# Kernel optimization log

Hardware: AMD Instinct MI355X
Metric: run time of the kernel (lower is better)

## Reference

```python
import jax, jax.numpy as jnp
import numpy as np

N = 100000      # nodes
MUL_IN = 256    # multiplicity of 0e and 1o in irreps_in ('256x0e + 256x1o')
MUL_H = 64      # multiplicity in MLP_irreps ('64x0e + 64x1o')
# irreps_nonlin = (64+64)x0e (scalars + gates) + 64x1o (gated)


def setup_inputs() -> dict:
    key = jax.random.key(0)
    k0, k1, k2, k3, k4 = jax.random.split(key, 5)
    # e3nn flat layout: [scalars (256), vectors (256*3, as (mul,3) flattened)]
    x = jax.random.normal(k0, (N, MUL_IN * 4), dtype=jnp.float32)
    # linear_1 block weights (e3nn Linear: randn init, output scaled by 1/sqrt(fan_in))
    w1_s = jax.random.normal(k1, (MUL_IN, 2 * MUL_H), dtype=jnp.float32)  # 0e->0e (scalars+gates)
    w1_v = jax.random.normal(k2, (MUL_IN, MUL_H), dtype=jnp.float32)      # 1o->1o
    # linear_2 block weights: 64x0e->1x0e, 64x1o->1x1o
    w2_s = jax.random.normal(k3, (MUL_H, 1), dtype=jnp.float32)
    w2_v = jax.random.normal(k4, (MUL_H, 1), dtype=jnp.float32)
    return {"x": x, "w1_s": w1_s, "w1_v": w1_v, "w2_s": w2_s, "w2_v": w2_v}


def reference(x, w1_s, w1_v, w2_s, w2_v):
    # ---- split input into irrep blocks ----
    xs = x[:, :MUL_IN]                          # [N, 256] 0e scalars
    xv = x[:, MUL_IN:].reshape(-1, MUL_IN, 3)   # [N, 256, 3] 1o vectors

    inv_in = np.float32(1.0 / np.sqrt(MUL_IN))
    # ---- linear_1: per-irrep block-diagonal matmuls (weight shared over m) ----
    h_s = (xs @ w1_s) * inv_in                              # [N, 128] scalars+gates
    h_v = jnp.einsum('nmi,mk->nki', xv, w1_v) * inv_in       # [N, 64, 3]

    # ---- Gate: act(scalars), act(gates) * gated_vectors ----
    scalars = h_s[:, :MUL_H]
    gates = h_s[:, MUL_H:]
    g_s = jax.nn.silu(scalars)                               # [N, 64]
    g_v = jax.nn.silu(gates)[:, :, None] * h_v               # [N, 64, 3]

    inv_h = np.float32(1.0 / np.sqrt(MUL_H))
    # ---- linear_2: 64x0e -> 1x0e, 64x1o -> 1x1o ----
    out_s = (g_s @ w2_s) * inv_h                             # [N, 1]
    out_v = jnp.einsum('nmi,mk->nki', g_v, w2_v).reshape(-1, 3) * inv_h  # [N, 3]
    return jnp.concatenate([out_s, out_v], axis=1)           # [N, 4] = 1x0e + 1x1o
```

## Files before the change

### kernel.cpp

```cpp
#include <hip/hip_runtime.h>
#include <hip/hip_bf16.h>
#include <math.h>

#define N_ROWS  100000
#define NT_ROW  6250

typedef __attribute__((ext_vector_type(8))) short bf16x8;
typedef __attribute__((ext_vector_type(4))) float f32x4;

__device__ __forceinline__ float silu_f(float v) {
    return v * (1.0f / (1.0f + __expf(-v)));
}
__device__ __forceinline__ short f2bf(float f) {
    union { __hip_bfloat16 h; short s; } u;
    u.h = __float2bfloat16(f);
    return u.s;
}
__device__ __forceinline__ void stage16(const float* g, float* l) {
    __builtin_amdgcn_global_load_lds(
        (const __attribute__((address_space(1))) unsigned int*)g,
        (__attribute__((address_space(3))) unsigned int*)l,
        16, 0, 0);
}

__global__ __launch_bounds__(64)
void prep_wT(const float* __restrict__ w1_s, const float* __restrict__ w1_v,
             unsigned short* __restrict__ wTf)
{
    const int tp = blockIdx.x;
    const int t = tp >> 3, p = tp & 7;
    const int lane = threadIdx.x;
    const int l15 = lane & 15, lq = lane >> 4;
    const float* src  = (t < 8) ? w1_s : w1_v;
    const int    strd = (t < 8) ? 128 : 64;
    const int    scol = (t < 8) ? (t * 16 + l15) : (((t - 8) & 3) * 16 + l15);
    const int    k0   = 32 * p + 8 * lq;
    unsigned short o[8];
    #pragma unroll
    for (int e = 0; e < 8; ++e)
        o[e] = (unsigned short)f2bf(src[(k0 + e) * strd + scol]);
    *(ushort4*)(wTf + (size_t)tp * 512 + lane * 8)     = make_ushort4(o[0], o[1], o[2], o[3]);
    *(ushort4*)(wTf + (size_t)tp * 512 + lane * 8 + 4) = make_ushort4(o[4], o[5], o[6], o[7]);
}

__global__ __launch_bounds__(256, 2)
void ndr_mfma_kernel(const float* __restrict__ x,
                     const unsigned short* __restrict__ wTf,
                     const float* __restrict__ w2_s,
                     const float* __restrict__ w2_v,
                     float* __restrict__ out)
{
    __shared__ float lds[2][4][2048];

    const int lane = threadIdx.x & 63;
    const int wid  = threadIdx.x >> 6;
    const int rt   = blockIdx.x * 4 + wid;
    if (rt >= NT_ROW) return;
    const int l15 = lane & 15, lq = lane >> 4;
    const long long n0 = (long long)rt * 16;

    const int sub = lane >> 5, slot = lane & 31;
    const float* sp[8];
    int sstep[8];
    #pragma unroll
    for (int j = 0; j < 8; ++j) {
        const int row = 2 * j + sub;
        const int g   = slot ^ (row & 7);
        const int isxs = (g < 8);
        const int f0  = isxs ? 4 * g : 256 + 4 * (g - 8);
        sstep[j] = isxs ? 32 : 96;
        sp[j] = x + (n0 + row) * 1024 + f0;
    }

    f32x4 acc[20];
    #pragma unroll
    for (int t = 0; t < 20; ++t) acc[t] = (f32x4){0.f, 0.f, 0.f, 0.f};

    const char* wbase = (const char*)wTf + lane * 16;

    #pragma unroll
    for (int j = 0; j < 8; ++j) stage16(sp[j],            &lds[0][wid][j * 256]);
    #pragma unroll
    for (int j = 0; j < 8; ++j) stage16(sp[j] + sstep[j], &lds[1][wid][j * 256]);

    const int r7 = l15 & 7;
    const float* rb0 = &lds[0][wid][l15 * 128];
    const float* rb1 = &lds[1][wid][l15 * 128];

    #pragma unroll 1
    for (int p = 0; p < 8; ++p) {
        if (p < 7) asm volatile("s_waitcnt vmcnt(8)" ::: "memory");
        else       asm volatile("s_waitcnt vmcnt(0)" ::: "memory");

        const float* rb = (p & 1) ? rb1 : rb0;
        float4 s0 = *(const float4*)(rb + 4 * (( 2 * lq     ) ^ r7));
        float4 s1 = *(const float4*)(rb + 4 * (( 2 * lq + 1 ) ^ r7));
        float4 v0 = *(const float4*)(rb + 4 * ((8 + 6 * lq + 0) ^ r7));
        float4 v1 = *(const float4*)(rb + 4 * ((8 + 6 * lq + 1) ^ r7));
        float4 v2 = *(const float4*)(rb + 4 * ((8 + 6 * lq + 2) ^ r7));
        float4 v3 = *(const float4*)(rb + 4 * ((8 + 6 * lq + 3) ^ r7));
        float4 v4 = *(const float4*)(rb + 4 * ((8 + 6 * lq + 4) ^ r7));
        float4 v5 = *(const float4*)(rb + 4 * ((8 + 6 * lq + 5) ^ r7));

        const float xs[8]  = {s0.x, s0.y, s0.z, s0.w, s1.x, s1.y, s1.z, s1.w};
        const float xv[24] = {v0.x, v0.y, v0.z, v0.w, v1.x, v1.y, v1.z, v1.w,
                              v2.x, v2.y, v2.z, v2.w, v3.x, v3.y, v3.z, v3.w,
                              v4.x, v4.y, v4.z, v4.w, v5.x, v5.y, v5.z, v5.w};
        bf16x8 a_s, a_v0, a_v1, a_v2;
        #pragma unroll
        for (int e = 0; e < 8; ++e) {
            a_s[e]  = f2bf(xs[e]);
            a_v0[e] = f2bf(xv[3 * e + 0]);
            a_v1[e] = f2bf(xv[3 * e + 1]);
            a_v2[e] = f2bf(xv[3 * e + 2]);
        }

        bf16x8 bf[20];
        #pragma unroll
        for (int t = 0; t < 20; ++t)
            bf[t] = *(const bf16x8*)(wbase + (size_t)p * 1024 + (size_t)t * 8192);

        if (p + 2 < 8) {
            asm volatile("s_waitcnt lgkmcnt(0)" ::: "memory");
            #pragma unroll
            for (int j = 0; j < 8; ++j)
                stage16(sp[j] + (p + 2) * sstep[j], &lds[p & 1][wid][j * 256]);
        }

        #pragma unroll
        for (int t = 0; t < 20; ++t) {
            const bf16x8 a = (t < 8) ? a_s : (t < 12) ? a_v0
                            : (t < 16) ? a_v1 : a_v2;
            acc[t] = __builtin_amdgcn_mfma_f32_16x16x32_bf16(a, bf[t], acc[t], 0, 0, 0);
        }
    }

    const float inv_in = 0.0625f, inv_h = 0.125f;
    float w2sv[4], w2vv[4];
    #pragma unroll
    for (int u = 0; u < 4; ++u) {
        w2sv[u] = w2_s[u * 16 + l15];
        w2vv[u] = w2_v[u * 16 + l15];
    }
    #pragma unroll
    for (int j = 0; j < 4; ++j) {
        float ps = 0.f, pv0 = 0.f, pv1 = 0.f, pv2 = 0.f;
        #pragma unroll
        for (int u = 0; u < 4; ++u) {
            float hs = acc[u][j]     * inv_in;
            float hg = acc[4 + u][j] * inv_in;
            float gg = silu_f(hg);
            ps  += silu_f(hs) * w2sv[u];
            pv0 += gg * (acc[8  + u][j] * inv_in) * w2vv[u];
            pv1 += gg * (acc[12 + u][j] * inv_in) * w2vv[u];
            pv2 += gg * (acc[16 + u][j] * inv_in) * w2vv[u];
        }
        #pragma unroll
        for (int off = 1; off <= 8; off <<= 1) {
            ps  += __shfl_xor(ps,  off, 64);
            pv0 += __shfl_xor(pv0, off, 64);
            pv1 += __shfl_xor(pv1, off, 64);
            pv2 += __shfl_xor(pv2, off, 64);
        }
        if (l15 == 0) {
            long long n = n0 + lq * 4 + j;
            *(float4*)(out + n * 4) =
                make_float4(ps * inv_h, pv0 * inv_h, pv1 * inv_h, pv2 * inv_h);
        }
    }
}

extern "C" void kernel_launch(void* const* d_in, const int* in_sizes, int n_in,
                              void* d_out, int out_size, void* d_ws, size_t ws_size,
                              hipStream_t stream) {
    const float* x    = (const float*)d_in[0];
    const float* w1_s = (const float*)d_in[1];
    const float* w1_v = (const float*)d_in[2];
    const float* w2_s = (const float*)d_in[3];
    const float* w2_v = (const float*)d_in[4];
    float* out = (float*)d_out;
    unsigned short* wTf = (unsigned short*)d_ws;

    prep_wT<<<160, 64, 0, stream>>>(w1_s, w1_v, wTf);
    int blocks = (NT_ROW + 3) / 4;
    ndr_mfma_kernel<<<blocks, 256, 0, stream>>>(x, wTf, w2_s, w2_v, out);
}
```

Measured before the change: 109.2 us.

## Split each 16-row tile across four waves by output column group

Each block now handles one 16-row tile instead of four. The four waves share one double-buffered LDS staging of x, and each wave computes only a quarter of the hidden columns (5 MFMA accumulators instead of 20). Partial linear_2 sums are combined across waves through LDS before the output is written. This cuts register use and raises occupancy (launch bounds 4), at the cost of block-wide barriers every step, an extra cross-wave reduction, and four times as many blocks.

```diff
diff --git a/kernel.cpp b/kernel.cpp
--- a/kernel.cpp
+++ b/kernel.cpp
@@ -43,58 +43,60 @@
     *(ushort4*)(wTf + (size_t)tp * 512 + lane * 8 + 4) = make_ushort4(o[4], o[5], o[6], o[7]);
 }
 
-__global__ __launch_bounds__(256, 2)
+__global__ __launch_bounds__(256, 4)
 void ndr_mfma_kernel(const float* __restrict__ x,
                      const unsigned short* __restrict__ wTf,
                      const float* __restrict__ w2_s,
                      const float* __restrict__ w2_v,
                      float* __restrict__ out)
 {
-    __shared__ float lds[2][4][2048];
+    __shared__ float  lds[2][16][128];
+    __shared__ float4 red[4][16];
 
     const int lane = threadIdx.x & 63;
     const int wid  = threadIdx.x >> 6;
-    const int rt   = blockIdx.x * 4 + wid;
-    if (rt >= NT_ROW) return;
-    const int l15 = lane & 15, lq = lane >> 4;
-    const long long n0 = (long long)rt * 16;
+    const int l15  = lane & 15, lq = lane >> 4;
+    const long long n0 = (long long)blockIdx.x * 16;
+
+    const float w2sv = w2_s[16 * wid + l15];
+    const float w2vv = w2_v[16 * wid + l15];
 
     const int sub = lane >> 5, slot = lane & 31;
-    const float* sp[8];
-    int sstep[8];
+    const float* sp[2];
+    int sstep[2];
     #pragma unroll
-    for (int j = 0; j < 8; ++j) {
+    for (int jj = 0; jj < 2; ++jj) {
+        const int j   = 2 * wid + jj;
         const int row = 2 * j + sub;
         const int g   = slot ^ (row & 7);
         const int isxs = (g < 8);
-        const int f0  = isxs ? 4 * g : 256 + 4 * (g - 8);
-        sstep[j] = isxs ? 32 : 96;
-        sp[j] = x + (n0 + row) * 1024 + f0;
+        sstep[jj] = isxs ? 32 : 96;
+        sp[jj] = x + (n0 + row) * 1024 + (isxs ? 4 * g : 256 + 4 * (g - 8));
     }
 
-    f32x4 acc[20];
+    f32x4 acc[5];
     #pragma unroll
-    for (int t = 0; t < 20; ++t) acc[t] = (f32x4){0.f, 0.f, 0.f, 0.f};
+    for (int t = 0; t < 5; ++t) acc[t] = (f32x4){0.f, 0.f, 0.f, 0.f};
 
     const char* wbase = (const char*)wTf + lane * 16;
 
     #pragma unroll
-    for (int j = 0; j < 8; ++j) stage16(sp[j],            &lds[0][wid][j * 256]);
+    for (int jj = 0; jj < 2; ++jj)
+        stage16(sp[jj],            &lds[0][0][0] + (2 * wid + jj) * 256);
     #pragma unroll
-    for (int j = 0; j < 8; ++j) stage16(sp[j] + sstep[j], &lds[1][wid][j * 256]);
+    for (int jj = 0; jj < 2; ++jj)
+        stage16(sp[jj] + sstep[jj], &lds[1][0][0] + (2 * wid + jj) * 256);
 
     const int r7 = l15 & 7;
-    const float* rb0 = &lds[0][wid][l15 * 128];
-    const float* rb1 = &lds[1][wid][l15 * 128];
 
     #pragma unroll 1
     for (int p = 0; p < 8; ++p) {
-        if (p < 7) asm volatile("s_waitcnt vmcnt(8)" ::: "memory");
-        else       asm volatile("s_waitcnt vmcnt(0)" ::: "memory");
+        asm volatile("s_waitcnt vmcnt(2)" ::: "memory");
+        __builtin_amdgcn_s_barrier();
 
-        const float* rb = (p & 1) ? rb1 : rb0;
-        float4 s0 = *(const float4*)(rb + 4 * (( 2 * lq     ) ^ r7));
-        float4 s1 = *(const float4*)(rb + 4 * (( 2 * lq + 1 ) ^ r7));
+        const float* rb = &lds[p & 1][l15][0];
+        float4 s0 = *(const float4*)(rb + 4 * ((2 * lq    ) ^ r7));
+        float4 s1 = *(const float4*)(rb + 4 * ((2 * lq + 1) ^ r7));
         float4 v0 = *(const float4*)(rb + 4 * ((8 + 6 * lq + 0) ^ r7));
         float4 v1 = *(const float4*)(rb + 4 * ((8 + 6 * lq + 1) ^ r7));
         float4 v2 = *(const float4*)(rb + 4 * ((8 + 6 * lq + 2) ^ r7));
@@ -115,46 +117,39 @@
             a_v2[e] = f2bf(xv[3 * e + 2]);
         }
 
-        bf16x8 bf[20];
+        bf16x8 bf[5];
         #pragma unroll
-        for (int t = 0; t < 20; ++t)
-            bf[t] = *(const bf16x8*)(wbase + (size_t)p * 1024 + (size_t)t * 8192);
+        for (int t = 0; t < 5; ++t)
+            bf[t] = *(const bf16x8*)(wbase + (size_t)(wid + 4 * t) * 8192
+                                           + (size_t)p * 1024);
+
+        asm volatile("s_waitcnt lgkmcnt(0)" ::: "memory");
+        __builtin_amdgcn_s_barrier();
 
         if (p + 2 < 8) {
-            asm volatile("s_waitcnt lgkmcnt(0)" ::: "memory");
             #pragma unroll
-            for (int j = 0; j < 8; ++j)
-                stage16(sp[j] + (p + 2) * sstep[j], &lds[p & 1][wid][j * 256]);
+            for (int jj = 0; jj < 2; ++jj)
+                stage16(sp[jj] + (p + 2) * sstep[jj],
+                        &lds[p & 1][0][0] + (2 * wid + jj) * 256);
         }
 
-        #pragma unroll
-        for (int t = 0; t < 20; ++t) {
-            const bf16x8 a = (t < 8) ? a_s : (t < 12) ? a_v0
-                            : (t < 16) ? a_v1 : a_v2;
-            acc[t] = __builtin_amdgcn_mfma_f32_16x16x32_bf16(a, bf[t], acc[t], 0, 0, 0);
-        }
+        acc[0] = __builtin_amdgcn_mfma_f32_16x16x32_bf16(a_s,  bf[0], acc[0], 0, 0, 0);
+        acc[1] = __builtin_amdgcn_mfma_f32_16x16x32_bf16(a_s,  bf[1], acc[1], 0, 0, 0);
+        acc[2] = __builtin_amdgcn_mfma_f32_16x16x32_bf16(a_v0, bf[2], acc[2], 0, 0, 0);
+        acc[3] = __builtin_amdgcn_mfma_f32_16x16x32_bf16(a_v1, bf[3], acc[3], 0, 0, 0);
+        acc[4] = __builtin_amdgcn_mfma_f32_16x16x32_bf16(a_v2, bf[4], acc[4], 0, 0, 0);
     }
 
     const float inv_in = 0.0625f, inv_h = 0.125f;
-    float w2sv[4], w2vv[4];
-    #pragma unroll
-    for (int u = 0; u < 4; ++u) {
-        w2sv[u] = w2_s[u * 16 + l15];
-        w2vv[u] = w2_v[u * 16 + l15];
-    }
     #pragma unroll
     for (int j = 0; j < 4; ++j) {
-        float ps = 0.f, pv0 = 0.f, pv1 = 0.f, pv2 = 0.f;
-        #pragma unroll
-        for (int u = 0; u < 4; ++u) {
-            float hs = acc[u][j]     * inv_in;
-            float hg = acc[4 + u][j] * inv_in;
-            float gg = silu_f(hg);
-            ps  += silu_f(hs) * w2sv[u];
-            pv0 += gg * (acc[8  + u][j] * inv_in) * w2vv[u];
-            pv1 += gg * (acc[12 + u][j] * inv_in) * w2vv[u];
-            pv2 += gg * (acc[16 + u][j] * inv_in) * w2vv[u];
-        }
+        float hs = acc[0][j] * inv_in;
+        float hg = acc[1][j] * inv_in;
+        float gg = silu_f(hg);
+        float ps  = silu_f(hs) * w2sv;
+        float pv0 = gg * (acc[2][j] * inv_in) * w2vv;
+        float pv1 = gg * (acc[3][j] * inv_in) * w2vv;
+        float pv2 = gg * (acc[4][j] * inv_in) * w2vv;
         #pragma unroll
         for (int off = 1; off <= 8; off <<= 1) {
             ps  += __shfl_xor(ps,  off, 64);
@@ -162,11 +157,18 @@
             pv1 += __shfl_xor(pv1, off, 64);
             pv2 += __shfl_xor(pv2, off, 64);
         }
-        if (l15 == 0) {
-            long long n = n0 + lq * 4 + j;
-            *(float4*)(out + n * 4) =
-                make_float4(ps * inv_h, pv0 * inv_h, pv1 * inv_h, pv2 * inv_h);
-        }
+        if (l15 == 0)
+            red[wid][lq * 4 + j] = make_float4(ps, pv0, pv1, pv2);
+    }
+    __syncthreads();
+    if (wid == 0 && lane < 16) {
+        float4 a = red[0][lane], b = red[1][lane],
+               c = red[2][lane], d = red[3][lane];
+        float4 o = make_float4((a.x + b.x + c.x + d.x) * inv_h,
+                               (a.y + b.y + c.y + d.y) * inv_h,
+                               (a.z + b.z + c.z + d.z) * inv_h,
+                               (a.w + b.w + c.w + d.w) * inv_h);
+        *(float4*)(out + (n0 + lane) * 4) = o;
     }
 }
 
@@ -182,6 +184,5 @@
     unsigned short* wTf = (unsigned short*)d_ws;
 
     prep_wT<<<160, 64, 0, stream>>>(w1_s, w1_v, wTf);
-    int blocks = (NT_ROW + 3) / 4;
-    ndr_mfma_kernel<<<blocks, 256, 0, stream>>>(x, wTf, w2_s, w2_v, out);
+    ndr_mfma_kernel<<<NT_ROW, 256, 0, stream>>>(x, wTf, w2_s, w2_v, out);
 }
```

Result: slower. 112.4 us (+2.9%).
